# Kernel tuning notes

Measured on AMD Instinct MI355X. Metric: run time of the kernel, lower is better.

## Reference

```python
import jax, jax.numpy as jnp
import numpy as np

B, S, D, H, DFF = 4, 2048, 768, 12, 3072
DH = D // H  # 64
EPS = 1e-5
SQRT_DK = float(np.sqrt(DH))


def layer_norm(x, gamma, beta):
    mu = jnp.mean(x, axis=-1, keepdims=True)
    var = jnp.mean((x - mu) ** 2, axis=-1, keepdims=True)
    return (x - mu) / jnp.sqrt(var + EPS) * gamma + beta


def attention_block(x, Wq, Wv, gamma, beta, mask):
    # NOTE: faithful to source quirks: k and v BOTH come from the V projection
    # (self.K is unused), and softmax is over dim=2 (the QUERY axis) as in
    # nn.Softmax(dim=2) applied to a (B, H, Sq, Sk) tensor.
    b, s, d = x.shape
    q = (x @ Wq).reshape(b, s, H, DH).transpose(0, 2, 1, 3)   # (B,H,S,DH)
    kv = (x @ Wv).reshape(b, s, H, DH).transpose(0, 2, 1, 3)  # (B,H,S,DH)
    w = jnp.einsum('bhqd,bhkd->bhqk', q, kv) / SQRT_DK        # (B,H,S,S)
    w = jnp.where(mask, -1e9, w)
    score = jax.nn.softmax(w, axis=2)  # dim=2 quirk (query axis)
    o = jnp.einsum('bhqk,bhkd->bhqd', score, kv)
    o = o.transpose(0, 2, 1, 3).reshape(b, s, d)
    return layer_norm(o + x, gamma, beta)


def feed_forward(x, W1, b1, W2, b2, gamma, beta):
    h = jax.nn.relu(x @ W1 + b1)
    return layer_norm(h @ W2 + b2 + x, gamma, beta)


def setup_inputs() -> dict:
    key = jax.random.key(0)
    ks = jax.random.split(key, 12)
    std = 1.0 / np.sqrt(D)
    x = jax.random.normal(ks[0], (B, S, D), dtype=jnp.float32)
    # causal mask: True = masked
    mask = jnp.triu(jnp.ones((S, S), dtype=bool), k=1)[None, None]
    return {
        'x': x,
        'mask': mask,
        'Wq1': jax.random.normal(ks[1], (D, D), jnp.float32) * std,
        'Wv1': jax.random.normal(ks[2], (D, D), jnp.float32) * std,
        'g1': jnp.ones((D,), jnp.float32),
        'be1': jnp.zeros((D,), jnp.float32),
        'Wq2': jax.random.normal(ks[3], (D, D), jnp.float32) * std,
        'Wv2': jax.random.normal(ks[4], (D, D), jnp.float32) * std,
        'g2': jnp.ones((D,), jnp.float32),
        'be2': jnp.zeros((D,), jnp.float32),
        'Wf1': jax.random.normal(ks[5], (D, DFF), jnp.float32) * std,
        'bf1': jnp.zeros((DFF,), jnp.float32),
        'Wf2': jax.random.normal(ks[6], (DFF, D), jnp.float32) * (1.0 / np.sqrt(DFF)),
        'bf2': jnp.zeros((D,), jnp.float32),
        'gf': jnp.ones((D,), jnp.float32),
        'bef': jnp.zeros((D,), jnp.float32),
    }


def reference(x, mask, Wq1, Wv1, g1, be1, Wq2, Wv2, g2, be2,
              Wf1, bf1, Wf2, bf2, gf, bef):
    x = attention_block(x, Wq1, Wv1, g1, be1, mask)
    # second block: mask is zeroed in the source (no masking)
    x = attention_block(x, Wq2, Wv2, g2, be2, jnp.zeros_like(mask))
    x = feed_forward(x, Wf1, bf1, Wf2, bf2, gf, bef)
    return x
```

## Files before the change

### kernel.cpp

```cpp
#include <hip/hip_runtime.h>

typedef __attribute__((ext_vector_type(8))) short short8;
typedef __attribute__((ext_vector_type(4))) float floatx4;
typedef __attribute__((ext_vector_type(4))) unsigned short ushort4v;

#define H_ 12
#define S_ 2048
#define D_ 768
#define DFF_ 3072
#define DH_ 64
#define BH_ 48
#define M_ 8192
#define QSCALE 0.180336880f

#if defined(__has_builtin)
#if __has_builtin(__builtin_amdgcn_exp2f)
#define EXP2V(x) __builtin_amdgcn_exp2f(x)
#endif
#if __has_builtin(__builtin_amdgcn_logf)
#define LOG2V(x) __builtin_amdgcn_logf(x)
#endif
#endif
#ifndef EXP2V
#define EXP2V(x) exp2f(x)
#endif
#ifndef LOG2V
#define LOG2V(x) log2f(x)
#endif

__device__ __forceinline__ unsigned short f2bf(float f) {
  union { float f; unsigned int u; } a; a.f = f;
  return (unsigned short)((a.u + 0x7FFFu + ((a.u >> 16) & 1u)) >> 16);
}
__device__ __forceinline__ unsigned int cvtpk_bf16(float lo, float hi) {
  unsigned int u;
  asm("v_cvt_pk_bf16_f32 %0, %1, %2" : "=v"(u) : "v"(lo), "v"(hi));
  return u;
}

__device__ __forceinline__ void glds16(const void* g, void* l) {
  __builtin_amdgcn_global_load_lds(
      (const __attribute__((address_space(1))) void*)(unsigned long long)(size_t)g,
      (__attribute__((address_space(3))) void*)(unsigned int)(size_t)l, 16, 0, 0);
}
__device__ __forceinline__ void glds4(const void* g, void* l) {
  __builtin_amdgcn_global_load_lds(
      (const __attribute__((address_space(1))) void*)(unsigned long long)(size_t)g,
      (__attribute__((address_space(3))) void*)(unsigned int)(size_t)l, 4, 0, 0);
}

__device__ __forceinline__ int swz8(int lin, int nwg) {
  return (lin & 7) * (nwg >> 3) + (lin >> 3);
}

__global__ __launch_bounds__(256) void cvt_bf16(const float* __restrict__ in,
                                                unsigned short* __restrict__ out) {
  size_t i = ((size_t)blockIdx.x * 256 + threadIdx.x) * 4;
  floatx4 v = *reinterpret_cast<const floatx4*>(in + i);
  ushort4v o;
  o[0] = f2bf(v[0]); o[1] = f2bf(v[1]); o[2] = f2bf(v[2]); o[3] = f2bf(v[3]);
  *reinterpret_cast<ushort4v*>(out + i) = o;
}

__global__ __launch_bounds__(256) void wtrans(const float* __restrict__ W,
                                              unsigned short* __restrict__ Wt,
                                              int K, int N) {
  __shared__ float t[64][65];
  const int n0 = blockIdx.x * 64, k0 = blockIdx.y * 64;
  const int tid = threadIdx.x;
#pragma unroll
  for (int i = 0; i < 16; ++i) {
    int idx = tid + 256 * i;
    int kl = idx >> 6, nl = idx & 63;
    t[kl][nl] = W[(size_t)(k0 + kl) * N + n0 + nl];
  }
  __syncthreads();
#pragma unroll
  for (int i = 0; i < 16; ++i) {
    int idx = tid + 256 * i;
    int nl = idx >> 6, kl = idx & 63;
    Wt[(size_t)(n0 + nl) * K + k0 + kl] = f2bf(t[kl][nl]);
  }
}

__global__ __launch_bounds__(256) void kvtrans(const unsigned short* __restrict__ KVb,
                                               unsigned short* __restrict__ KVTb) {
  __shared__ unsigned short t[64][72];
  const int kk0 = blockIdx.x * 64;
  const int bh = blockIdx.y, b = bh / H_, h = bh % H_;
  const size_t xbase = ((size_t)b * S_) * D_ + h * DH_;
  const int tid = threadIdx.x;
#pragma unroll
  for (int i = 0; i < 16; ++i) {
    int idx = tid + 256 * i;
    int kl = idx >> 6, d = idx & 63;
    t[kl][d] = KVb[xbase + (size_t)(kk0 + kl) * D_ + d];
  }
  __syncthreads();
  const size_t tb = (size_t)bh * DH_ * S_;
#pragma unroll
  for (int i = 0; i < 16; ++i) {
    int idx = tid + 256 * i;
    int d = idx >> 6, kl = idx & 63;
    KVTb[tb + (size_t)d * S_ + kk0 + kl] = t[kl][d];
  }
}

template <int EPI, int OUTBF>
__global__ __launch_bounds__(256, 2) void gemm128(const unsigned short* __restrict__ A,
                                                  const unsigned short* __restrict__ Bt,
                                                  const float* __restrict__ bias,
                                                  float scale, void* __restrict__ C0,
                                                  void* __restrict__ C1,
                                                  int M, int N, int K, int lda) {
  __shared__ unsigned short As[128 * 64];
  __shared__ unsigned short Bs[128 * 64];
  const int tid = threadIdx.x;
  const int l = tid & 63, w = tid >> 6;
  const int wm = w >> 1, wn = w & 1;
  const int lrow = l & 15, lk = l >> 4;
  int lin = (blockIdx.z * gridDim.y + blockIdx.y) * gridDim.x + blockIdx.x;
  int nwg = gridDim.x * gridDim.y * gridDim.z;
  int s = swz8(lin, nwg);
  int xt = s % gridDim.x;
  int rest = s / gridDim.x;
  int yt = rest % gridDim.y;
  int zt = rest / gridDim.y;
  const unsigned short* Ao = A + (size_t)zt * K;
  const unsigned short* Bo = Bt + (size_t)zt * K;
  const int m0 = yt * 128, n0 = xt * 128;
  floatx4 acc[4][4] = {};
  for (int k0 = 0; k0 < K; k0 += 64) {
    __syncthreads();
#pragma unroll
    for (int i = 0; i < 4; ++i) {
      int idx = w * 64 + i * 256 + l;
      int row = idx >> 3, c8 = idx & 7;
      int sc = (c8 ^ (row & 7)) << 3;
      glds16(Ao + (size_t)(m0 + row) * lda + k0 + sc, As + (size_t)(w * 64 + i * 256) * 8);
      glds16(Bo + (size_t)(n0 + row) * lda + k0 + sc, Bs + (size_t)(w * 64 + i * 256) * 8);
    }
    __syncthreads();
#pragma unroll
    for (int ks = 0; ks < 2; ++ks) {
      short8 af[4], bfr[4];
#pragma unroll
      for (int f = 0; f < 4; ++f) {
        int ar = wm * 64 + f * 16 + lrow;
        af[f] = *reinterpret_cast<const short8*>(
            &As[ar * 64 + (((ks * 4 + lk) ^ (ar & 7)) << 3)]);
        int br = wn * 64 + f * 16 + lrow;
        bfr[f] = *reinterpret_cast<const short8*>(
            &Bs[br * 64 + (((ks * 4 + lk) ^ (br & 7)) << 3)]);
      }
#pragma unroll
      for (int fm = 0; fm < 4; ++fm)
#pragma unroll
        for (int fn = 0; fn < 4; ++fn)
          acc[fm][fn] =
              __builtin_amdgcn_mfma_f32_16x16x32_bf16(af[fm], bfr[fn], acc[fm][fn], 0, 0, 0);
    }
  }
#pragma unroll
  for (int fm = 0; fm < 4; ++fm) {
#pragma unroll
    for (int fn = 0; fn < 4; ++fn) {
      int col = n0 + wn * 64 + fn * 16 + lrow;
#pragma unroll
      for (int r = 0; r < 4; ++r) {
        int row = m0 + wm * 64 + fm * 16 + lk * 4 + r;
        float v = acc[fm][fn][r];
        if (EPI == 3) {
          if (col < 768)
            ((unsigned short*)C0)[(size_t)row * 768 + col] = f2bf(v * scale);
          else
            ((unsigned short*)C1)[(size_t)row * 768 + col - 768] = f2bf(v);
        } else {
          v = v * scale + ((EPI > 0) ? bias[col] : 0.0f);
          if (EPI == 1) v = fmaxf(v, 0.0f);
          void* Cz = zt ? C1 : C0;
          if (OUTBF) ((unsigned short*)Cz)[(size_t)row * N + col] = f2bf(v);
          else ((float*)Cz)[(size_t)row * N + col] = v;
        }
      }
    }
  }
}

template <bool CAUSAL>
__global__ __launch_bounds__(256, 4) void colsum(const unsigned short* __restrict__ Qb,
                                                 const unsigned short* __restrict__ KVb,
                                                 float* __restrict__ lnl) {
  __shared__ unsigned short kvs[64 * 64];
  __shared__ float lred[4][64];
  const int tid = threadIdx.x;
  const int l = tid & 63, w = tid >> 6;
  const int lrow = l & 15, lk = l >> 4;
  const int sw = swz8(blockIdx.x, 32 * BH_);
  const int bh = sw >> 5, kt = sw & 31;
  const int kk0 = kt * 64;
  const int b = bh / H_, h = bh % H_;
  const size_t xbase = ((size_t)b * S_) * D_ + h * DH_;
#pragma unroll
  for (int i = 0; i < 2; ++i) {
    int idx = w * 64 + i * 256 + l;
    int row = idx >> 3, c8 = idx & 7;
    glds16(KVb + xbase + (size_t)(kk0 + row) * D_ + ((c8 ^ (row & 7)) << 3),
           kvs + (size_t)(w * 64 + i * 256) * 8);
  }
  __syncthreads();
  short8 bkv[4][2];
#pragma unroll
  for (int kkf = 0; kkf < 4; ++kkf)
#pragma unroll
    for (int s = 0; s < 2; ++s) {
      int br = kkf * 16 + lrow;
      bkv[kkf][s] = *reinterpret_cast<const short8*>(
          &kvs[br * 64 + (((s * 4 + lk) ^ (br & 7)) << 3)]);
    }
  float lrun[4] = {0.0f, 0.0f, 0.0f, 0.0f};
  const int qbase = CAUSAL ? kk0 : 0;
  const int ntiles = (S_ - qbase) >> 4;
  short8 aqn[2];
  if (w < ntiles) {
    const int q0 = qbase + w * 16;
#pragma unroll
    for (int s = 0; s < 2; ++s)
      aqn[s] = *reinterpret_cast<const short8*>(
          &Qb[xbase + (size_t)(q0 + lrow) * D_ + s * 32 + lk * 8]);
  }
  for (int t = w; t < ntiles; t += 4) {
    const int q0 = qbase + t * 16;
    const bool maskt = CAUSAL && (q0 < kk0 + 64);
    short8 aq0 = aqn[0], aq1 = aqn[1];
    if (t + 4 < ntiles) {
      const int qn = qbase + (t + 4) * 16;
#pragma unroll
      for (int s = 0; s < 2; ++s)
        aqn[s] = *reinterpret_cast<const short8*>(
            &Qb[xbase + (size_t)(qn + lrow) * D_ + s * 32 + lk * 8]);
    }
#pragma unroll
    for (int kkf = 0; kkf < 4; ++kkf) {
      floatx4 sf = {};
      sf = __builtin_amdgcn_mfma_f32_16x16x32_bf16(aq0, bkv[kkf][0], sf, 0, 0, 0);
      sf = __builtin_amdgcn_mfma_f32_16x16x32_bf16(aq1, bkv[kkf][1], sf, 0, 0, 0);
      const int kkg = kk0 + kkf * 16 + lrow;
      float lacc = 0.0f;
      if (maskt) {
#pragma unroll
        for (int r = 0; r < 4; ++r) {
          int qg = q0 + lk * 4 + r;
          lacc += (kkg <= qg) ? EXP2V(sf[r]) : 0.0f;
        }
      } else {
#pragma unroll
        for (int r = 0; r < 4; ++r) lacc += EXP2V(sf[r]);
      }
      lrun[kkf] += lacc;
    }
  }
#pragma unroll
  for (int kkf = 0; kkf < 4; ++kkf) {
    float lv = lrun[kkf];
    lv += __shfl_xor(lv, 16, 64);
    lv += __shfl_xor(lv, 32, 64);
    if (l < 16) lred[w][kkf * 16 + l] = lv;
  }
  __syncthreads();
  if (tid < 64) {
    float lv = lred[0][tid] + lred[1][tid] + lred[2][tid] + lred[3][tid];
    lnl[(size_t)bh * S_ + kk0 + tid] = -LOG2V(lv);
  }
}

template <bool CAUSAL>
__global__ __launch_bounds__(256, 3) void attnpv(const unsigned short* __restrict__ Qb,
                                                 const unsigned short* __restrict__ KVb,
                                                 const unsigned short* __restrict__ KVTb,
                                                 const float* __restrict__ lnl,
                                                 float* __restrict__ Opre) {
  __shared__ unsigned short kvs[2][64 * 64];
  __shared__ unsigned short kvts[2][64 * 64];
  __shared__ float slnl[2][4][64];
  __shared__ unsigned short ps[4][32 * 64];
  const int tid = threadIdx.x;
  const int l = tid & 63, w = tid >> 6;
  const int lrow = l & 15, lk = l >> 4;
  const int sw = swz8(blockIdx.x, 16 * BH_);
  const int bh = sw >> 4, qtr = sw & 15;
  const int qt = CAUSAL ? (15 - qtr) : qtr;
  const int q0 = qt * 128;
  const int wr = w * 32;
  const int b = bh / H_, h = bh % H_;
  const size_t xbase = ((size_t)b * S_) * D_ + h * DH_;
  const size_t tbase = (size_t)bh * DH_ * S_;
  const float* lnlb = lnl + (size_t)bh * S_;

  auto STAGE = [&](int buf, int t) {
    const int kk0 = t * 64;
#pragma unroll
    for (int i = 0; i < 2; ++i) {
      int idx = w * 64 + i * 256 + l;
      int row = idx >> 3, c8 = idx & 7;
      int sc = (c8 ^ (row & 7)) << 3;
      glds16(KVb + xbase + (size_t)(kk0 + row) * D_ + sc,
             &kvs[buf][(size_t)(w * 64 + i * 256) * 8]);
      glds16(KVTb + tbase + (size_t)row * S_ + kk0 + sc,
             &kvts[buf][(size_t)(w * 64 + i * 256) * 8]);
    }
    glds4(lnlb + kk0 + l, &slnl[buf][w][0]);
  };

  short8 aq[2][2];
#pragma unroll
  for (int fm = 0; fm < 2; ++fm)
#pragma unroll
    for (int s = 0; s < 2; ++s)
      aq[fm][s] = *reinterpret_cast<const short8*>(
          &Qb[xbase + (size_t)(q0 + wr + fm * 16 + lrow) * D_ + s * 32 + lk * 8]);
  floatx4 ao[2][4] = {};
  const int nkk = CAUSAL ? 2 * (qt + 1) : (S_ / 64);

  STAGE(0, 0);
  int cur = 0;
  for (int t = 0; t < nkk; ++t) {
    const int kk0 = t * 64;
    const bool maskt = CAUSAL && (kk0 + 64 > q0);
    if (t + 1 < nkk) {
      STAGE(cur ^ 1, t + 1);
      __builtin_amdgcn_sched_barrier(0);
      asm volatile("s_waitcnt vmcnt(5)" ::: "memory");
    } else {
      __builtin_amdgcn_sched_barrier(0);
      asm volatile("s_waitcnt vmcnt(0)" ::: "memory");
    }
    __builtin_amdgcn_s_barrier();
    __builtin_amdgcn_sched_barrier(0);
#pragma unroll
    for (int kkf = 0; kkf < 4; ++kkf) {
      const int br = kkf * 16 + lrow;
      short8 b0 =
          *reinterpret_cast<const short8*>(&kvs[cur][br * 64 + ((lk ^ (br & 7)) << 3)]);
      short8 b1 =
          *reinterpret_cast<const short8*>(&kvs[cur][br * 64 + (((4 + lk) ^ (br & 7)) << 3)]);
      const floatx4 nl4 =
          *reinterpret_cast<const floatx4*>(&slnl[cur][w][kkf * 16 + lk * 4]);
      const int kkbase = kk0 + kkf * 16 + lk * 4;
#pragma unroll
      for (int fm = 0; fm < 2; ++fm) {
        floatx4 sf = nl4;
        sf = __builtin_amdgcn_mfma_f32_16x16x32_bf16(b0, aq[fm][0], sf, 0, 0, 0);
        sf = __builtin_amdgcn_mfma_f32_16x16x32_bf16(b1, aq[fm][1], sf, 0, 0, 0);
        float p0 = EXP2V(sf[0]);
        float p1 = EXP2V(sf[1]);
        float p2 = EXP2V(sf[2]);
        float p3 = EXP2V(sf[3]);
        if (maskt) {
          const int qg = q0 + wr + fm * 16 + lrow;
          p0 = (kkbase + 0 <= qg) ? p0 : 0.0f;
          p1 = (kkbase + 1 <= qg) ? p1 : 0.0f;
          p2 = (kkbase + 2 <= qg) ? p2 : 0.0f;
          p3 = (kkbase + 3 <= qg) ? p3 : 0.0f;
        }
        unsigned int u0 = cvtpk_bf16(p0, p1);
        unsigned int u1 = cvtpk_bf16(p2, p3);
        const int rowq = fm * 16 + lrow;
        unsigned short* pb =
            &ps[w][rowq * 64 + ((((kkf << 1) + (lk >> 1)) ^ (lrow & 7)) << 3) +
                   ((lk & 1) << 2)];
        *reinterpret_cast<unsigned int*>(pb) = u0;
        *reinterpret_cast<unsigned int*>(pb + 2) = u1;
      }
    }
    short8 pa[2][2];
#pragma unroll
    for (int fm = 0; fm < 2; ++fm)
#pragma unroll
      for (int s2 = 0; s2 < 2; ++s2)
        pa[fm][s2] = *reinterpret_cast<const short8*>(
            &ps[w][(fm * 16 + lrow) * 64 + (((s2 * 4 + lk) ^ (lrow & 7)) << 3)]);
    __builtin_amdgcn_s_setprio(1);
#pragma unroll
    for (int dn = 0; dn < 4; ++dn) {
#pragma unroll
      for (int s2 = 0; s2 < 2; ++s2) {
        const int br2 = dn * 16 + lrow;
        short8 bv = *reinterpret_cast<const short8*>(
            &kvts[cur][br2 * 64 + (((s2 * 4 + lk) ^ (br2 & 7)) << 3)]);
#pragma unroll
        for (int fm = 0; fm < 2; ++fm)
          ao[fm][dn] =
              __builtin_amdgcn_mfma_f32_16x16x32_bf16(pa[fm][s2], bv, ao[fm][dn], 0, 0, 0);
      }
    }
    __builtin_amdgcn_s_setprio(0);
    __builtin_amdgcn_sched_barrier(0);
    __builtin_amdgcn_s_barrier();
    __builtin_amdgcn_sched_barrier(0);
    cur ^= 1;
  }
#pragma unroll
  for (int fm = 0; fm < 2; ++fm)
#pragma unroll
    for (int dn = 0; dn < 4; ++dn)
#pragma unroll
      for (int r = 0; r < 4; ++r)
        Opre[xbase + (size_t)(q0 + wr + fm * 16 + lk * 4 + r) * D_ + dn * 16 + lrow] =
            ao[fm][dn][r];
}

template <bool WRITEBF, bool TWO, bool BIAS>
__global__ __launch_bounds__(256) void ln_kernel(const float* __restrict__ pre,
                                                 const float* __restrict__ pre2,
                                                 const float* __restrict__ bias,
                                                 const float* __restrict__ res,
                                                 const float* __restrict__ gam,
                                                 const float* __restrict__ bet,
                                                 float* __restrict__ outf,
                                                 unsigned short* __restrict__ outb) {
  const int w = threadIdx.x >> 6, l = threadIdx.x & 63;
  const int row = blockIdx.x * 4 + w;
  const size_t base = (size_t)row * D_;
  floatx4 v[3];
  float s = 0.0f;
#pragma unroll
  for (int j = 0; j < 3; ++j) {
    int i = j * 256 + l * 4;
    floatx4 t = *reinterpret_cast<const floatx4*>(&pre[base + i]);
    floatx4 rv = *reinterpret_cast<const floatx4*>(&res[base + i]);
#pragma unroll
    for (int e = 0; e < 4; ++e) t[e] += rv[e];
    if (TWO) {
      floatx4 t2 = *reinterpret_cast<const floatx4*>(&pre2[base + i]);
#pragma unroll
      for (int e = 0; e < 4; ++e) t[e] += t2[e];
    }
    if (BIAS) {
      floatx4 bv = *reinterpret_cast<const floatx4*>(&bias[i]);
#pragma unroll
      for (int e = 0; e < 4; ++e) t[e] += bv[e];
    }
    v[j] = t;
#pragma unroll
    for (int e = 0; e < 4; ++e) s += t[e];
  }
#pragma unroll
  for (int off = 32; off; off >>= 1) s += __shfl_xor(s, off, 64);
  const float mu = s * (1.0f / 768.0f);
  float vs = 0.0f;
#pragma unroll
  for (int j = 0; j < 3; ++j)
#pragma unroll
    for (int e = 0; e < 4; ++e) { float d = v[j][e] - mu; vs += d * d; }
#pragma unroll
  for (int off = 32; off; off >>= 1) vs += __shfl_xor(vs, off, 64);
  const float rstd = rsqrtf(vs * (1.0f / 768.0f) + 1e-5f);
#pragma unroll
  for (int j = 0; j < 3; ++j) {
    int i = j * 256 + l * 4;
    floatx4 gv = *reinterpret_cast<const floatx4*>(&gam[i]);
    floatx4 bev = *reinterpret_cast<const floatx4*>(&bet[i]);
    floatx4 o;
#pragma unroll
    for (int e = 0; e < 4; ++e) o[e] = (v[j][e] - mu) * rstd * gv[e] + bev[e];
    *reinterpret_cast<floatx4*>(&outf[base + i]) = o;
    if (WRITEBF) {
      ushort4v ob;
#pragma unroll
      for (int e = 0; e < 4; ++e) ob[e] = f2bf(o[e]);
      *reinterpret_cast<ushort4v*>(&outb[base + i]) = ob;
    }
  }
}

extern "C" void kernel_launch(void* const* d_in, const int* in_sizes, int n_in,
                              void* d_out, int out_size, void* d_ws, size_t ws_size,
                              hipStream_t stream) {
  const float* x = (const float*)d_in[0];
  const float* Wq1 = (const float*)d_in[2];
  const float* Wv1 = (const float*)d_in[3];
  const float* g1 = (const float*)d_in[4];
  const float* be1 = (const float*)d_in[5];
  const float* Wq2 = (const float*)d_in[6];
  const float* Wv2 = (const float*)d_in[7];
  const float* g2 = (const float*)d_in[8];
  const float* be2 = (const float*)d_in[9];
  const float* Wf1 = (const float*)d_in[10];
  const float* bf1 = (const float*)d_in[11];
  const float* Wf2 = (const float*)d_in[12];
  const float* bf2 = (const float*)d_in[13];
  const float* gf = (const float*)d_in[14];
  const float* bef = (const float*)d_in[15];

  char* ws = (char*)d_ws;
  size_t off = 0;
  auto alloc = [&](size_t bytes) -> void* {
    void* p = ws + off;
    off += (bytes + 255) & ~(size_t)255;
    return p;
  };
  unsigned short* xb = (unsigned short*)alloc((size_t)M_ * D_ * 2);
  unsigned short* qb = (unsigned short*)alloc((size_t)M_ * D_ * 2);
  unsigned short* kvb = (unsigned short*)alloc((size_t)M_ * D_ * 2);
  unsigned short* kvtb = (unsigned short*)alloc((size_t)BH_ * DH_ * S_ * 2);
  float* lnl = (float*)alloc((size_t)BH_ * S_ * 4);
  float* preA = (float*)alloc((size_t)M_ * D_ * 4);
  float* xcur = (float*)alloc((size_t)M_ * D_ * 4);
  unsigned short* hb = (unsigned short*)alloc((size_t)M_ * DFF_ * 2);
  unsigned short* wqv1t = (unsigned short*)alloc((size_t)D_ * 1536 * 2);
  unsigned short* wqv2t = (unsigned short*)alloc((size_t)D_ * 1536 * 2);
  unsigned short* wf1t = (unsigned short*)alloc((size_t)D_ * DFF_ * 2);
  unsigned short* wf2t = (unsigned short*)alloc((size_t)D_ * DFF_ * 2);
  float* preB = (float*)qb;
  if (off > ws_size) return;

  const dim3 blk(256);
  cvt_bf16<<<dim3((M_ * D_) / 1024), blk, 0, stream>>>(x, xb);
  wtrans<<<dim3(12, 12), blk, 0, stream>>>(Wq1, wqv1t, D_, D_);
  wtrans<<<dim3(12, 12), blk, 0, stream>>>(Wv1, wqv1t + (size_t)768 * 768, D_, D_);
  wtrans<<<dim3(12, 12), blk, 0, stream>>>(Wq2, wqv2t, D_, D_);
  wtrans<<<dim3(12, 12), blk, 0, stream>>>(Wv2, wqv2t + (size_t)768 * 768, D_, D_);
  wtrans<<<dim3(48, 12), blk, 0, stream>>>(Wf1, wf1t, D_, DFF_);
  wtrans<<<dim3(12, 48), blk, 0, stream>>>(Wf2, wf2t, DFF_, D_);

  const dim3 gqkv(12, 64);
  const dim3 gkvt(S_ / 64, BH_);

  gemm128<3, 1><<<gqkv, blk, 0, stream>>>(xb, wqv1t, nullptr, QSCALE, qb, kvb, M_, 1536, D_, D_);
  kvtrans<<<gkvt, blk, 0, stream>>>(kvb, kvtb);
  colsum<true><<<dim3(32 * BH_), blk, 0, stream>>>(qb, kvb, lnl);
  attnpv<true><<<dim3(16 * BH_), blk, 0, stream>>>(qb, kvb, kvtb, lnl, preA);
  ln_kernel<true, false, false><<<dim3(M_ / 4), blk, 0, stream>>>(preA, nullptr, nullptr, x, g1,
                                                                  be1, xcur, xb);

  gemm128<3, 1><<<gqkv, blk, 0, stream>>>(xb, wqv2t, nullptr, QSCALE, qb, kvb, M_, 1536, D_, D_);
  kvtrans<<<gkvt, blk, 0, stream>>>(kvb, kvtb);
  colsum<false><<<dim3(32 * BH_), blk, 0, stream>>>(qb, kvb, lnl);
  attnpv<false><<<dim3(16 * BH_), blk, 0, stream>>>(qb, kvb, kvtb, lnl, preA);
  ln_kernel<true, false, false><<<dim3(M_ / 4), blk, 0, stream>>>(preA, nullptr, nullptr, xcur,
                                                                  g2, be2, xcur, xb);

  gemm128<1, 1><<<dim3(24, 64), blk, 0, stream>>>(xb, wf1t, bf1, 1.0f, hb, nullptr, M_, DFF_,
                                                  D_, D_);
  gemm128<0, 0><<<dim3(6, 64, 2), blk, 0, stream>>>(hb, wf2t, nullptr, 1.0f, preA, preB, M_, D_,
                                                    DFF_ / 2, DFF_);
  ln_kernel<false, true, true><<<dim3(M_ / 4), blk, 0, stream>>>(preA, preB, bf2, xcur, gf, bef,
                                                                 (float*)d_out, nullptr);
}
```

Before: 468.7 us.

## Double-buffer GEMM LDS tiles with async prefetch and merge P stores

```diff
diff --git a/kernel.cpp b/kernel.cpp
--- a/kernel.cpp
+++ b/kernel.cpp
@@ -113,8 +113,8 @@
                                                   float scale, void* __restrict__ C0,
                                                   void* __restrict__ C1,
                                                   int M, int N, int K, int lda) {
-  __shared__ unsigned short As[128 * 64];
-  __shared__ unsigned short Bs[128 * 64];
+  __shared__ unsigned short As[2][128 * 64];
+  __shared__ unsigned short Bs[2][128 * 64];
   const int tid = threadIdx.x;
   const int l = tid & 63, w = tid >> 6;
   const int wm = w >> 1, wn = w & 1;
@@ -129,18 +129,35 @@
   const unsigned short* Ao = A + (size_t)zt * K;
   const unsigned short* Bo = Bt + (size_t)zt * K;
   const int m0 = yt * 128, n0 = xt * 128;
-  floatx4 acc[4][4] = {};
-  for (int k0 = 0; k0 < K; k0 += 64) {
-    __syncthreads();
+
+  auto STAGE = [&](int buf, int k0) {
 #pragma unroll
     for (int i = 0; i < 4; ++i) {
       int idx = w * 64 + i * 256 + l;
       int row = idx >> 3, c8 = idx & 7;
       int sc = (c8 ^ (row & 7)) << 3;
-      glds16(Ao + (size_t)(m0 + row) * lda + k0 + sc, As + (size_t)(w * 64 + i * 256) * 8);
-      glds16(Bo + (size_t)(n0 + row) * lda + k0 + sc, Bs + (size_t)(w * 64 + i * 256) * 8);
-    }
-    __syncthreads();
+      glds16(Ao + (size_t)(m0 + row) * lda + k0 + sc,
+             &As[buf][(size_t)(w * 64 + i * 256) * 8]);
+      glds16(Bo + (size_t)(n0 + row) * lda + k0 + sc,
+             &Bs[buf][(size_t)(w * 64 + i * 256) * 8]);
+    }
+  };
+
+  floatx4 acc[4][4] = {};
+  const int nk = K / 64;
+  STAGE(0, 0);
+  int cur = 0;
+  for (int t = 0; t < nk; ++t) {
+    if (t + 1 < nk) {
+      STAGE(cur ^ 1, (t + 1) * 64);
+      __builtin_amdgcn_sched_barrier(0);
+      asm volatile("s_waitcnt vmcnt(8)" ::: "memory");
+    } else {
+      __builtin_amdgcn_sched_barrier(0);
+      asm volatile("s_waitcnt vmcnt(0)" ::: "memory");
+    }
+    __builtin_amdgcn_s_barrier();
+    __builtin_amdgcn_sched_barrier(0);
 #pragma unroll
     for (int ks = 0; ks < 2; ++ks) {
       short8 af[4], bfr[4];
@@ -148,10 +165,10 @@
       for (int f = 0; f < 4; ++f) {
         int ar = wm * 64 + f * 16 + lrow;
         af[f] = *reinterpret_cast<const short8*>(
-            &As[ar * 64 + (((ks * 4 + lk) ^ (ar & 7)) << 3)]);
+            &As[cur][ar * 64 + (((ks * 4 + lk) ^ (ar & 7)) << 3)]);
         int br = wn * 64 + f * 16 + lrow;
         bfr[f] = *reinterpret_cast<const short8*>(
-            &Bs[br * 64 + (((ks * 4 + lk) ^ (br & 7)) << 3)]);
+            &Bs[cur][br * 64 + (((ks * 4 + lk) ^ (br & 7)) << 3)]);
       }
 #pragma unroll
       for (int fm = 0; fm < 4; ++fm)
@@ -160,6 +177,10 @@
           acc[fm][fn] =
               __builtin_amdgcn_mfma_f32_16x16x32_bf16(af[fm], bfr[fn], acc[fm][fn], 0, 0, 0);
     }
+    __builtin_amdgcn_sched_barrier(0);
+    __builtin_amdgcn_s_barrier();
+    __builtin_amdgcn_sched_barrier(0);
+    cur ^= 1;
   }
 #pragma unroll
   for (int fm = 0; fm < 4; ++fm) {
@@ -369,8 +390,8 @@
         unsigned short* pb =
             &ps[w][rowq * 64 + ((((kkf << 1) + (lk >> 1)) ^ (lrow & 7)) << 3) +
                    ((lk & 1) << 2)];
-        *reinterpret_cast<unsigned int*>(pb) = u0;
-        *reinterpret_cast<unsigned int*>(pb + 2) = u1;
+        *reinterpret_cast<unsigned long long*>(pb) =
+            (unsigned long long)u0 | ((unsigned long long)u1 << 32);
       }
     }
     short8 pa[2][2];
```

Measured after the change: 473.3 us. Within noise of the previous version (+1.0%).

## Pre-pack KV into MFMA fragment layout and load directly into registers

Applied to the files above, without the earlier changes.

```diff
diff --git a/kernel.cpp b/kernel.cpp
--- a/kernel.cpp
+++ b/kernel.cpp
@@ -84,9 +84,11 @@
 }
 
 __global__ __launch_bounds__(256) void kvtrans(const unsigned short* __restrict__ KVb,
-                                               unsigned short* __restrict__ KVTb) {
+                                               unsigned short* __restrict__ KVTb,
+                                               unsigned short* __restrict__ kfb) {
   __shared__ unsigned short t[64][72];
-  const int kk0 = blockIdx.x * 64;
+  const int kt = blockIdx.x;
+  const int kk0 = kt * 64;
   const int bh = blockIdx.y, b = bh / H_, h = bh % H_;
   const size_t xbase = ((size_t)b * S_) * D_ + h * DH_;
   const int tid = threadIdx.x;
@@ -103,6 +105,16 @@
     int idx = tid + 256 * i;
     int d = idx >> 6, kl = idx & 63;
     KVTb[tb + (size_t)d * S_ + kk0 + kl] = t[kl][d];
+  }
+  const size_t obase = ((size_t)bh * 32 + kt) * 4096;
+#pragma unroll
+  for (int i = 0; i < 2; ++i) {
+    int idx = tid + 256 * i;
+    int fi = idx >> 6, ll = idx & 63;
+    int kkf = fi >> 1, s = fi & 1;
+    short8 v =
+        *reinterpret_cast<const short8*>(&t[kkf * 16 + (ll & 15)][s * 32 + (ll >> 4) * 8]);
+    *reinterpret_cast<short8*>(&kfb[obase + (size_t)fi * 512 + ll * 8]) = v;
   }
 }
 
@@ -189,9 +201,8 @@
 
 template <bool CAUSAL>
 __global__ __launch_bounds__(256, 4) void colsum(const unsigned short* __restrict__ Qb,
-                                                 const unsigned short* __restrict__ KVb,
+                                                 const unsigned short* __restrict__ kfb,
                                                  float* __restrict__ lnl) {
-  __shared__ unsigned short kvs[64 * 64];
   __shared__ float lred[4][64];
   const int tid = threadIdx.x;
   const int l = tid & 63, w = tid >> 6;
@@ -201,23 +212,14 @@
   const int kk0 = kt * 64;
   const int b = bh / H_, h = bh % H_;
   const size_t xbase = ((size_t)b * S_) * D_ + h * DH_;
-#pragma unroll
-  for (int i = 0; i < 2; ++i) {
-    int idx = w * 64 + i * 256 + l;
-    int row = idx >> 3, c8 = idx & 7;
-    glds16(KVb + xbase + (size_t)(kk0 + row) * D_ + ((c8 ^ (row & 7)) << 3),
-           kvs + (size_t)(w * 64 + i * 256) * 8);
-  }
-  __syncthreads();
+  const unsigned short* kfT = kfb + ((size_t)bh * 32 + kt) * 4096;
   short8 bkv[4][2];
 #pragma unroll
   for (int kkf = 0; kkf < 4; ++kkf)
 #pragma unroll
-    for (int s = 0; s < 2; ++s) {
-      int br = kkf * 16 + lrow;
-      bkv[kkf][s] = *reinterpret_cast<const short8*>(
-          &kvs[br * 64 + (((s * 4 + lk) ^ (br & 7)) << 3)]);
-    }
+    for (int s = 0; s < 2; ++s)
+      bkv[kkf][s] =
+          *reinterpret_cast<const short8*>(&kfT[(size_t)(kkf * 2 + s) * 512 + l * 8]);
   float lrun[4] = {0.0f, 0.0f, 0.0f, 0.0f};
   const int qbase = CAUSAL ? kk0 : 0;
   const int ntiles = (S_ - qbase) >> 4;
@@ -276,11 +278,10 @@
 
 template <bool CAUSAL>
 __global__ __launch_bounds__(256, 3) void attnpv(const unsigned short* __restrict__ Qb,
-                                                 const unsigned short* __restrict__ KVb,
+                                                 const unsigned short* __restrict__ kfb,
                                                  const unsigned short* __restrict__ KVTb,
                                                  const float* __restrict__ lnl,
                                                  float* __restrict__ Opre) {
-  __shared__ unsigned short kvs[2][64 * 64];
   __shared__ unsigned short kvts[2][64 * 64];
   __shared__ float slnl[2][4][64];
   __shared__ unsigned short ps[4][32 * 64];
@@ -296,6 +297,7 @@
   const size_t xbase = ((size_t)b * S_) * D_ + h * DH_;
   const size_t tbase = (size_t)bh * DH_ * S_;
   const float* lnlb = lnl + (size_t)bh * S_;
+  const unsigned short* kfB = kfb + (size_t)bh * 32 * 4096;
 
   auto STAGE = [&](int buf, int t) {
     const int kk0 = t * 64;
@@ -304,8 +306,6 @@
       int idx = w * 64 + i * 256 + l;
       int row = idx >> 3, c8 = idx & 7;
       int sc = (c8 ^ (row & 7)) << 3;
-      glds16(KVb + xbase + (size_t)(kk0 + row) * D_ + sc,
-             &kvs[buf][(size_t)(w * 64 + i * 256) * 8]);
       glds16(KVTb + tbase + (size_t)row * S_ + kk0 + sc,
              &kvts[buf][(size_t)(w * 64 + i * 256) * 8]);
     }
@@ -327,31 +327,31 @@
   for (int t = 0; t < nkk; ++t) {
     const int kk0 = t * 64;
     const bool maskt = CAUSAL && (kk0 + 64 > q0);
+    short8 kc[8];
+#pragma unroll
+    for (int fi = 0; fi < 8; ++fi)
+      kc[fi] =
+          *reinterpret_cast<const short8*>(&kfB[((size_t)t * 8 + fi) * 512 + l * 8]);
     if (t + 1 < nkk) {
       STAGE(cur ^ 1, t + 1);
       __builtin_amdgcn_sched_barrier(0);
-      asm volatile("s_waitcnt vmcnt(5)" ::: "memory");
+      asm volatile("s_waitcnt vmcnt(11)" ::: "memory");
     } else {
       __builtin_amdgcn_sched_barrier(0);
-      asm volatile("s_waitcnt vmcnt(0)" ::: "memory");
+      asm volatile("s_waitcnt vmcnt(8)" ::: "memory");
     }
     __builtin_amdgcn_s_barrier();
     __builtin_amdgcn_sched_barrier(0);
 #pragma unroll
     for (int kkf = 0; kkf < 4; ++kkf) {
-      const int br = kkf * 16 + lrow;
-      short8 b0 =
-          *reinterpret_cast<const short8*>(&kvs[cur][br * 64 + ((lk ^ (br & 7)) << 3)]);
-      short8 b1 =
-          *reinterpret_cast<const short8*>(&kvs[cur][br * 64 + (((4 + lk) ^ (br & 7)) << 3)]);
       const floatx4 nl4 =
           *reinterpret_cast<const floatx4*>(&slnl[cur][w][kkf * 16 + lk * 4]);
       const int kkbase = kk0 + kkf * 16 + lk * 4;
 #pragma unroll
       for (int fm = 0; fm < 2; ++fm) {
         floatx4 sf = nl4;
-        sf = __builtin_amdgcn_mfma_f32_16x16x32_bf16(b0, aq[fm][0], sf, 0, 0, 0);
-        sf = __builtin_amdgcn_mfma_f32_16x16x32_bf16(b1, aq[fm][1], sf, 0, 0, 0);
+        sf = __builtin_amdgcn_mfma_f32_16x16x32_bf16(kc[kkf * 2 + 0], aq[fm][0], sf, 0, 0, 0);
+        sf = __builtin_amdgcn_mfma_f32_16x16x32_bf16(kc[kkf * 2 + 1], aq[fm][1], sf, 0, 0, 0);
         float p0 = EXP2V(sf[0]);
         float p1 = EXP2V(sf[1]);
         float p2 = EXP2V(sf[2]);
@@ -504,6 +504,7 @@
   unsigned short* qb = (unsigned short*)alloc((size_t)M_ * D_ * 2);
   unsigned short* kvb = (unsigned short*)alloc((size_t)M_ * D_ * 2);
   unsigned short* kvtb = (unsigned short*)alloc((size_t)BH_ * DH_ * S_ * 2);
+  unsigned short* kfb = (unsigned short*)alloc((size_t)BH_ * 32 * 4096 * 2);
   float* lnl = (float*)alloc((size_t)BH_ * S_ * 4);
   float* preA = (float*)alloc((size_t)M_ * D_ * 4);
   float* xcur = (float*)alloc((size_t)M_ * D_ * 4);
@@ -528,16 +529,16 @@
   const dim3 gkvt(S_ / 64, BH_);
 
   gemm128<3, 1><<<gqkv, blk, 0, stream>>>(xb, wqv1t, nullptr, QSCALE, qb, kvb, M_, 1536, D_, D_);
-  kvtrans<<<gkvt, blk, 0, stream>>>(kvb, kvtb);
-  colsum<true><<<dim3(32 * BH_), blk, 0, stream>>>(qb, kvb, lnl);
-  attnpv<true><<<dim3(16 * BH_), blk, 0, stream>>>(qb, kvb, kvtb, lnl, preA);
+  kvtrans<<<gkvt, blk, 0, stream>>>(kvb, kvtb, kfb);
+  colsum<true><<<dim3(32 * BH_), blk, 0, stream>>>(qb, kfb, lnl);
+  attnpv<true><<<dim3(16 * BH_), blk, 0, stream>>>(qb, kfb, kvtb, lnl, preA);
   ln_kernel<true, false, false><<<dim3(M_ / 4), blk, 0, stream>>>(preA, nullptr, nullptr, x, g1,
                                                                   be1, xcur, xb);
 
   gemm128<3, 1><<<gqkv, blk, 0, stream>>>(xb, wqv2t, nullptr, QSCALE, qb, kvb, M_, 1536, D_, D_);
-  kvtrans<<<gkvt, blk, 0, stream>>>(kvb, kvtb);
-  colsum<false><<<dim3(32 * BH_), blk, 0, stream>>>(qb, kvb, lnl);
-  attnpv<false><<<dim3(16 * BH_), blk, 0, stream>>>(qb, kvb, kvtb, lnl, preA);
+  kvtrans<<<gkvt, blk, 0, stream>>>(kvb, kvtb, kfb);
+  colsum<false><<<dim3(32 * BH_), blk, 0, stream>>>(qb, kfb, lnl);
+  attnpv<false><<<dim3(16 * BH_), blk, 0, stream>>>(qb, kfb, kvtb, lnl, preA);
   ln_kernel<true, false, false><<<dim3(M_ / 4), blk, 0, stream>>>(preA, nullptr, nullptr, xcur,
                                                                   g2, be2, xcur, xb);
 
```

Result: no change. 465.0 us, median of 2 (-0.8%).
